# Kernel tuning notes

Hardware: AMD Instinct MI355X
Metric: run time of the kernel (lower is better)

Reference implementation:

```python
import jax, jax.numpy as jnp
import numpy as np

DIM_MODEL = 512
SCALE = DIM_MODEL ** (-0.5)


def setup_inputs() -> dict:
    key = jax.random.key(0)
    k1, k2, k3, k4 = jax.random.split(key, 4)
    n, d, c_q, h, w = 64, 512, 512, 8, 128
    t = h * w
    query = jax.random.normal(k1, (n, d, c_q), dtype=jnp.float32)
    key_t = jax.random.normal(k2, (n, d, t), dtype=jnp.float32)
    value = jax.random.normal(k3, (n, d, t), dtype=jnp.float32)
    # valid ratios in [0.5, 1.0] so every sample keeps a non-empty valid width
    valid_ratios = 0.5 + 0.5 * jax.random.uniform(k4, (n,), dtype=jnp.float32)
    return {"query": query, "key": key_t, "value": value,
            "valid_ratios": valid_ratios, "h": h, "w": w}


def reference(query, key, value, valid_ratios, h, w):
    # query: [n, d, c]; key: [n, d, t]; value: [n, d, t]; t = h*w
    q = jnp.transpose(query, (0, 2, 1))                 # [n, c, d]
    logits = jnp.einsum('ncd,ndt->nct', q, key) * SCALE  # [n, c, t]
    n, c, t = logits.shape
    # per-sample valid width: min(w, int(w * ratio + 0.5)) (truncation == floor for positive)
    valid_width = jnp.minimum(w, jnp.floor(w * valid_ratios + 0.5)).astype(jnp.int32)  # [n]
    col = jnp.arange(w, dtype=jnp.int32)
    col_mask = col[None, :] < valid_width[:, None]       # [n, w]
    logits = logits.reshape(n, c, h, w)
    logits = jnp.where(col_mask[:, None, None, :], logits, -jnp.inf)
    weights = jax.nn.softmax(logits.reshape(n, c, t), axis=2)  # [n, c, t]
    v = jnp.transpose(value, (0, 2, 1))                  # [n, t, d]
    glimpse = jnp.einsum('nct,ntd->ncd', weights, v)     # [n, c, d]
    return jnp.transpose(glimpse, (0, 2, 1))             # [n, d, c]
```

## Files before the change

kernel.cpp:

```cpp
#include <hip/hip_runtime.h>
#include <hip/hip_bf16.h>

#define NS   64
#define DDIM 512
#define CDIM 512
#define TDIM 1024
#define WW   128
#define CB   64
#define TBLK 128
#define BK   64
#define SCALE 0.04419417382415922f

typedef __attribute__((ext_vector_type(4)))  float f32x4;
typedef __attribute__((ext_vector_type(16))) float f32x16;
typedef __attribute__((ext_vector_type(4)))  short s16x4;
typedef __attribute__((ext_vector_type(8)))  short s16x8;

#define LGKM_BARRIER() asm volatile("s_waitcnt lgkmcnt(0)\n\ts_barrier" ::: "memory")

__device__ __forceinline__ unsigned short f2bf(float f) {
  unsigned int b = __float_as_uint(f);
  return (unsigned short)((b + 0x7FFFu + ((b >> 16) & 1u)) >> 16);
}
__device__ __forceinline__ float bf2f(unsigned short u) {
  return __uint_as_float(((unsigned int)u) << 16);
}

#define AS_OFF 0
#define BS_OFF 8704
#define PS_OFF 26112
#define ZA_OFF 43008
#define IZ_OFF 43264
#define SMEM_BYTES 43520

struct QKRegs { f32x4 q0, q1, ka0, ka1, kb0, kb1; };
struct VRegs  { f32x4 a0, a1, b0, b1; };

__device__ __forceinline__ void issue_qk(QKRegs& r,
                                         const float* __restrict__ qbase,
                                         const float* __restrict__ kbase,
                                         int k0, int t0,
                                         int a_mg, int a_kq, int b_tg, int b_kq) {
  const float* gq = qbase + (size_t)(k0 + 2 * a_kq) * CDIM + 4 * a_mg;
  r.q0 = *(const f32x4*)gq;
  r.q1 = *(const f32x4*)(gq + CDIM);
  const float* gk0 = kbase + (size_t)(k0 + 2 * b_kq) * TDIM + t0 + 4 * b_tg;
  const float* gk1 = gk0 + (size_t)32 * TDIM;
  r.ka0 = *(const f32x4*)gk0;
  r.ka1 = *(const f32x4*)(gk0 + TDIM);
  r.kb0 = *(const f32x4*)gk1;
  r.kb1 = *(const f32x4*)(gk1 + TDIM);
}

__device__ __forceinline__ void issue_v(VRegs& r,
                                        const float* __restrict__ vrow0,
                                        int ks, int lhi) {
  const int kk = ks * 16 + 8 * lhi;
  const float* vp0 = vrow0 + kk;
  r.a0 = *(const f32x4*)vp0;
  r.a1 = *(const f32x4*)(vp0 + 4);
  const float* vp1 = vp0 + (size_t)32 * TDIM;
  r.b0 = *(const f32x4*)vp1;
  r.b1 = *(const f32x4*)(vp1 + 4);
}

__device__ __forceinline__ s16x8 cvt_bv(const f32x4& x0, const f32x4& x1) {
  s16x8 bv;
  bv[0] = (short)f2bf(x0[0]); bv[1] = (short)f2bf(x0[1]);
  bv[2] = (short)f2bf(x0[2]); bv[3] = (short)f2bf(x0[3]);
  bv[4] = (short)f2bf(x1[0]); bv[5] = (short)f2bf(x1[1]);
  bv[6] = (short)f2bf(x1[2]); bv[7] = (short)f2bf(x1[3]);
  return bv;
}

__global__ __launch_bounds__(512, 1)
void attn_fused_kernel(const float* __restrict__ query,
                       const float* __restrict__ key,
                       const float* __restrict__ value,
                       const float* __restrict__ ratios,
                       float* __restrict__ out)
{
  __shared__ __align__(16) char smem[SMEM_BYTES];
  unsigned short* As = (unsigned short*)(smem + AS_OFF);
  unsigned short* Bs = (unsigned short*)(smem + BS_OFF);
  unsigned short* Ps = (unsigned short*)(smem + PS_OFF);
  float* Zacc = (float*)(smem + ZA_OFF);
  float* invZ = (float*)(smem + IZ_OFF);
  float* Obuf = (float*)(smem + AS_OFF);

  const int lin  = blockIdx.x + (int)gridDim.x * blockIdx.y;
  const int n    = 8 * (lin & 7) + (lin >> 6);
  const int c0   = ((lin >> 3) & 7) * CB;

  const int tid  = threadIdx.x;
  const int wave = tid >> 6;
  const int lane = tid & 63;
  const int l31  = lane & 31;
  const int lhi  = lane >> 5;

  float r = ratios[n];
  int vw = (int)floorf(128.0f * r + 0.5f);
  if (vw > 128) vw = 128;

  if (tid < 64) Zacc[tid] = 0.0f;

  const float* qbase = query + (size_t)n * DDIM * CDIM + c0;
  const float* kbase = key   + (size_t)n * DDIM * TDIM;
  const float* vbase = value + (size_t)n * DDIM * TDIM;

  f32x16 o_acc[2][2];
  #pragma unroll
  for (int a = 0; a < 2; ++a)
    #pragma unroll
    for (int b = 0; b < 2; ++b)
      #pragma unroll
      for (int i = 0; i < 16; ++i) o_acc[a][b][i] = 0.0f;

  const int p1_ct = wave & 1;
  const int p1_tt = wave >> 1;
  const int a_mg = tid & 15, a_kq = tid >> 4;
  const int b_tg = tid & 31, b_kq = tid >> 5;
  const float* vrow0_base = vbase + (size_t)(64 * wave + l31) * TDIM;

  QKRegs buf[2];
  issue_qk(buf[0], qbase, kbase, 0,  0, a_mg, a_kq, b_tg, b_kq);
  issue_qk(buf[1], qbase, kbase, BK, 0, a_mg, a_kq, b_tg, b_kq);

  LGKM_BARRIER();

  for (int tb = 0; tb < 8; ++tb) {
    const int t0 = tb * TBLK;
    f32x16 s_acc;
    #pragma unroll
    for (int i = 0; i < 16; ++i) s_acc[i] = 0.0f;

    #pragma unroll
    for (int kit = 0; kit < 8; ++kit) {
      const int g = tb * 8 + kit;
      QKRegs& rb = buf[kit & 1];

      LGKM_BARRIER();

      #pragma unroll
      for (int j = 0; j < 4; ++j) {
        unsigned int pk = (unsigned int)f2bf(rb.q0[j]) | ((unsigned int)f2bf(rb.q1[j]) << 16);
        *(unsigned int*)&As[(4 * a_mg + j) * 68 + 2 * a_kq] = pk;
      }
      #pragma unroll
      for (int j = 0; j < 4; ++j) {
        unsigned int p0 = (unsigned int)f2bf(rb.ka0[j]) | ((unsigned int)f2bf(rb.ka1[j]) << 16);
        unsigned int p1 = (unsigned int)f2bf(rb.kb0[j]) | ((unsigned int)f2bf(rb.kb1[j]) << 16);
        *(unsigned int*)&Bs[(4 * b_tg + j) * 68 + 2 * b_kq]      = p0;
        *(unsigned int*)&Bs[(4 * b_tg + j) * 68 + 2 * b_kq + 32] = p1;
      }

      {
        int gg = g + 2; if (gg > 63) gg = 63;
        issue_qk(rb, qbase, kbase, (gg & 7) * BK, (gg >> 3) * TBLK,
                 a_mg, a_kq, b_tg, b_kq);
      }

      LGKM_BARRIER();

      const int arow = (32 * p1_ct + l31) * 68;
      const int brow = (32 * p1_tt + l31) * 68;
      #pragma unroll
      for (int ks = 0; ks < 4; ++ks) {
        const int koff = ks * 16 + 8 * lhi;
        s16x4 a0 = *(const s16x4*)&As[arow + koff];
        s16x4 a1 = *(const s16x4*)&As[arow + koff + 4];
        s16x4 b0 = *(const s16x4*)&Bs[brow + koff];
        s16x4 b1 = *(const s16x4*)&Bs[brow + koff + 4];
        s16x8 av = __builtin_shufflevector(a0, a1, 0, 1, 2, 3, 4, 5, 6, 7);
        s16x8 bv = __builtin_shufflevector(b0, b1, 0, 1, 2, 3, 4, 5, 6, 7);
        s_acc = __builtin_amdgcn_mfma_f32_32x32x16_bf16(av, bv, s_acc, 0, 0, 0);
      }
    }

    {
      const int tcol = 32 * p1_tt + l31;
      const float pm = (tcol < vw) ? 1.0f : 0.0f;
      #pragma unroll
      for (int rg = 0; rg < 16; ++rg) {
        const int c_loc = 32 * p1_ct + (rg & 3) + 8 * (rg >> 2) + 4 * lhi;
        float p = pm * __expf(s_acc[rg] * SCALE);
        Ps[c_loc * 132 + tcol] = f2bf(p);
      }
    }
    LGKM_BARRIER();

    {
      const int zr = tid >> 3;
      const int zo = (tid & 7) * 16;
      float zs = 0.0f;
      #pragma unroll
      for (int j = 0; j < 16; ++j) zs += bf2f(Ps[zr * 132 + zo + j]);
      zs += __shfl_xor(zs, 1);
      zs += __shfl_xor(zs, 2);
      zs += __shfl_xor(zs, 4);
      if ((tid & 7) == 0) Zacc[zr] += zs;
    }

    {
      const float* vrow0 = vrow0_base + t0;
      VRegs vb[2];
      issue_v(vb[0], vrow0, 0, lhi);
      issue_v(vb[1], vrow0, 1, lhi);
      #pragma unroll
      for (int ks = 0; ks < 8; ++ks) {
        const int kk = ks * 16 + 8 * lhi;
        s16x8 pa[2];
        #pragma unroll
        for (int ci = 0; ci < 2; ++ci) {
          const int row = (32 * ci + l31) * 132;
          s16x4 x0 = *(const s16x4*)&Ps[row + kk];
          s16x4 x1 = *(const s16x4*)&Ps[row + kk + 4];
          pa[ci] = __builtin_shufflevector(x0, x1, 0, 1, 2, 3, 4, 5, 6, 7);
        }
        VRegs& vr = vb[ks & 1];
        s16x8 bv0 = cvt_bv(vr.a0, vr.a1);
        s16x8 bv1 = cvt_bv(vr.b0, vr.b1);
        if (ks < 6) issue_v(vr, vrow0, ks + 2, lhi);
        o_acc[0][0] = __builtin_amdgcn_mfma_f32_32x32x16_bf16(pa[0], bv0, o_acc[0][0], 0, 0, 0);
        o_acc[1][0] = __builtin_amdgcn_mfma_f32_32x32x16_bf16(pa[1], bv0, o_acc[1][0], 0, 0, 0);
        o_acc[0][1] = __builtin_amdgcn_mfma_f32_32x32x16_bf16(pa[0], bv1, o_acc[0][1], 0, 0, 0);
        o_acc[1][1] = __builtin_amdgcn_mfma_f32_32x32x16_bf16(pa[1], bv1, o_acc[1][1], 0, 0, 0);
      }
    }
  }

  LGKM_BARRIER();
  if (tid < 64) invZ[tid] = 1.0f / Zacc[tid];
  LGKM_BARRIER();

  float* outn = out + (size_t)n * DDIM * CDIM + c0;
  for (int ch = 0; ch < 4; ++ch) {
    if ((wave >> 1) == ch) {
      const int s = wave & 1;
      #pragma unroll
      for (int ci = 0; ci < 2; ++ci)
        #pragma unroll
        for (int dt = 0; dt < 2; ++dt)
          #pragma unroll
          for (int rg = 0; rg < 16; ++rg) {
            const int c_loc = 32 * ci + (rg & 3) + 8 * (rg >> 2) + 4 * lhi;
            const int ddl = 64 * s + 32 * dt + l31;
            Obuf[c_loc * 129 + ddl] = o_acc[ci][dt][rg] * invZ[c_loc];
          }
    }
    LGKM_BARRIER();
    {
      const int c = tid & 63;
      const int db = tid >> 6;
      #pragma unroll
      for (int p = 0; p < 16; ++p) {
        const int ddl = db + 8 * p;
        outn[(size_t)(128 * ch + ddl) * CDIM + c] = Obuf[c * 129 + ddl];
      }
    }
    LGKM_BARRIER();
  }
}

extern "C" void kernel_launch(void* const* d_in, const int* in_sizes, int n_in,
                              void* d_out, int out_size, void* d_ws, size_t ws_size,
                              hipStream_t stream) {
  const float* query  = (const float*)d_in[0];
  const float* key    = (const float*)d_in[1];
  const float* value  = (const float*)d_in[2];
  const float* ratios = (const float*)d_in[3];
  float* out = (float*)d_out;
  (void)in_sizes; (void)n_in; (void)out_size; (void)d_ws; (void)ws_size;
  dim3 grid(CDIM / CB, NS);
  attn_fused_kernel<<<grid, 512, 0, stream>>>(query, key, value, ratios, out);
}
```

Baseline: 545.3 us.

## Double-buffer QK LDS tiles, widen T block, accumulate softmax sums in registers

Doubles the T block from 128 to 256 so each wave computes two 32x32 score tiles per Q fragment, reusing the A operand. Q/K staging in LDS is now double-buffered, which drops one of the two barriers per k-iteration. The softmax denominator is accumulated in fp32 registers and reduced with shuffles at the end, replacing the per-block LDS re-read of the bf16 P tile. LDS use grows to about 119 KB and launch bounds now request 2 blocks per CU, which that LDS size likely cannot satisfy, so register pressure is capped with little occupancy in return.

```diff
diff --git a/kernel.cpp b/kernel.cpp
--- a/kernel.cpp
+++ b/kernel.cpp
@@ -1,13 +1,11 @@
 #include <hip/hip_runtime.h>
-#include <hip/hip_bf16.h>
 
 #define NS   64
 #define DDIM 512
 #define CDIM 512
 #define TDIM 1024
-#define WW   128
 #define CB   64
-#define TBLK 128
+#define TBLK 256
 #define BK   64
 #define SCALE 0.04419417382415922f
 
@@ -22,46 +20,32 @@
   unsigned int b = __float_as_uint(f);
   return (unsigned short)((b + 0x7FFFu + ((b >> 16) & 1u)) >> 16);
 }
-__device__ __forceinline__ float bf2f(unsigned short u) {
-  return __uint_as_float(((unsigned int)u) << 16);
-}
-
-#define AS_OFF 0
-#define BS_OFF 8704
-#define PS_OFF 26112
-#define ZA_OFF 43008
-#define IZ_OFF 43264
-#define SMEM_BYTES 43520
-
-struct QKRegs { f32x4 q0, q1, ka0, ka1, kb0, kb1; };
-struct VRegs  { f32x4 a0, a1, b0, b1; };
-
-__device__ __forceinline__ void issue_qk(QKRegs& r,
-                                         const float* __restrict__ qbase,
-                                         const float* __restrict__ kbase,
-                                         int k0, int t0,
-                                         int a_mg, int a_kq, int b_tg, int b_kq) {
-  const float* gq = qbase + (size_t)(k0 + 2 * a_kq) * CDIM + 4 * a_mg;
-  r.q0 = *(const f32x4*)gq;
-  r.q1 = *(const f32x4*)(gq + CDIM);
-  const float* gk0 = kbase + (size_t)(k0 + 2 * b_kq) * TDIM + t0 + 4 * b_tg;
-  const float* gk1 = gk0 + (size_t)32 * TDIM;
-  r.ka0 = *(const f32x4*)gk0;
-  r.ka1 = *(const f32x4*)(gk0 + TDIM);
-  r.kb0 = *(const f32x4*)gk1;
-  r.kb1 = *(const f32x4*)(gk1 + TDIM);
-}
-
-__device__ __forceinline__ void issue_v(VRegs& r,
-                                        const float* __restrict__ vrow0,
+__device__ __forceinline__ unsigned int pk2(float a, float b) {
+  return (unsigned int)f2bf(a) | ((unsigned int)f2bf(b) << 16);
+}
+
+#define AS_STRIDE 68
+#define BS_STRIDE 68
+#define PS_STRIDE 260
+#define AS0_OFF 0
+#define AS1_OFF 8704
+#define BS0_OFF 17408
+#define BS1_OFF 52224
+#define PS_OFF  87040
+#define ZP_OFF  120320
+#define IZ_OFF  121344
+#define SMEM_BYTES 121600
+
+struct Stage { f32x4 q0, q1, ka[4], kb[4]; };
+struct VRegs { f32x4 a0, a1, b0, b1; };
+
+__device__ __forceinline__ void issue_v(VRegs& r, const float* __restrict__ vrow,
                                         int ks, int lhi) {
   const int kk = ks * 16 + 8 * lhi;
-  const float* vp0 = vrow0 + kk;
-  r.a0 = *(const f32x4*)vp0;
-  r.a1 = *(const f32x4*)(vp0 + 4);
-  const float* vp1 = vp0 + (size_t)32 * TDIM;
-  r.b0 = *(const f32x4*)vp1;
-  r.b1 = *(const f32x4*)(vp1 + 4);
+  r.a0 = *(const f32x4*)(vrow + kk);
+  r.a1 = *(const f32x4*)(vrow + kk + 4);
+  r.b0 = *(const f32x4*)(vrow + (size_t)32 * TDIM + kk);
+  r.b1 = *(const f32x4*)(vrow + (size_t)32 * TDIM + kk + 4);
 }
 
 __device__ __forceinline__ s16x8 cvt_bv(const f32x4& x0, const f32x4& x1) {
@@ -73,7 +57,7 @@
   return bv;
 }
 
-__global__ __launch_bounds__(512, 1)
+__global__ __launch_bounds__(512, 2)
 void attn_fused_kernel(const float* __restrict__ query,
                        const float* __restrict__ key,
                        const float* __restrict__ value,
@@ -81,12 +65,14 @@
                        float* __restrict__ out)
 {
   __shared__ __align__(16) char smem[SMEM_BYTES];
-  unsigned short* As = (unsigned short*)(smem + AS_OFF);
-  unsigned short* Bs = (unsigned short*)(smem + BS_OFF);
+  unsigned short* Asbuf[2] = {(unsigned short*)(smem + AS0_OFF),
+                              (unsigned short*)(smem + AS1_OFF)};
+  unsigned short* Bsbuf[2] = {(unsigned short*)(smem + BS0_OFF),
+                              (unsigned short*)(smem + BS1_OFF)};
   unsigned short* Ps = (unsigned short*)(smem + PS_OFF);
-  float* Zacc = (float*)(smem + ZA_OFF);
-  float* invZ = (float*)(smem + IZ_OFF);
-  float* Obuf = (float*)(smem + AS_OFF);
+  float* Zpart = (float*)(smem + ZP_OFF);
+  float* invZ  = (float*)(smem + IZ_OFF);
+  float* Obuf  = (float*)smem;
 
   const int lin  = blockIdx.x + (int)gridDim.x * blockIdx.y;
   const int n    = 8 * (lin & 7) + (lin >> 6);
@@ -98,16 +84,22 @@
   const int l31  = lane & 31;
   const int lhi  = lane >> 5;
 
-  float r = ratios[n];
-  int vw = (int)floorf(128.0f * r + 0.5f);
+  float rr = ratios[n];
+  int vw = (int)floorf(128.0f * rr + 0.5f);
   if (vw > 128) vw = 128;
-
-  if (tid < 64) Zacc[tid] = 0.0f;
 
   const float* qbase = query + (size_t)n * DDIM * CDIM + c0;
   const float* kbase = key   + (size_t)n * DDIM * TDIM;
   const float* vbase = value + (size_t)n * DDIM * TDIM;
 
+  const int kpq = (tid & 7) + 8 * (tid >> 7);
+  const int cg  = (tid >> 3) & 15;
+  const int kpk = tid & 7;
+  const int tg  = tid >> 3;
+
+  const int ct  = wave & 1;
+  const int ttp = wave >> 1;
+
   f32x16 o_acc[2][2];
   #pragma unroll
   for (int a = 0; a < 2; ++a)
@@ -116,103 +108,108 @@
       #pragma unroll
       for (int i = 0; i < 16; ++i) o_acc[a][b][i] = 0.0f;
 
-  const int p1_ct = wave & 1;
-  const int p1_tt = wave >> 1;
-  const int a_mg = tid & 15, a_kq = tid >> 4;
-  const int b_tg = tid & 31, b_kq = tid >> 5;
-  const float* vrow0_base = vbase + (size_t)(64 * wave + l31) * TDIM;
-
-  QKRegs buf[2];
-  issue_qk(buf[0], qbase, kbase, 0,  0, a_mg, a_kq, b_tg, b_kq);
-  issue_qk(buf[1], qbase, kbase, BK, 0, a_mg, a_kq, b_tg, b_kq);
-
-  LGKM_BARRIER();
-
-  for (int tb = 0; tb < 8; ++tb) {
+  float z_loc[16];
+  #pragma unroll
+  for (int i = 0; i < 16; ++i) z_loc[i] = 0.0f;
+
+  Stage st;
+  auto issue_stage = [&](int g) {
+    const int k0 = (g & 7) * BK;
+    const int t0 = (g >> 3) * TBLK;
+    const float* gq = qbase + (size_t)(k0 + 2 * kpq) * CDIM + 4 * cg;
+    st.q0 = *(const f32x4*)gq;
+    st.q1 = *(const f32x4*)(gq + CDIM);
+    #pragma unroll
+    for (int i = 0; i < 4; ++i) {
+      const int d = k0 + 2 * (kpk + 8 * i);
+      const float* gk = kbase + (size_t)d * TDIM + t0 + 4 * tg;
+      st.ka[i] = *(const f32x4*)gk;
+      st.kb[i] = *(const f32x4*)(gk + TDIM);
+    }
+  };
+  auto write_stage = [&](int b) {
+    unsigned int* Au = (unsigned int*)Asbuf[b];
+    unsigned int* Bu = (unsigned int*)Bsbuf[b];
+    #pragma unroll
+    for (int j = 0; j < 4; ++j)
+      Au[(4 * cg + j) * (AS_STRIDE / 2) + kpq] = pk2(st.q0[j], st.q1[j]);
+    #pragma unroll
+    for (int i = 0; i < 4; ++i)
+      #pragma unroll
+      for (int j = 0; j < 4; ++j)
+        Bu[(4 * tg + j) * (BS_STRIDE / 2) + kpk + 8 * i] = pk2(st.ka[i][j], st.kb[i][j]);
+  };
+
+  issue_stage(0);
+  write_stage(0);
+  issue_stage(1);
+
+  const int arow  = (32 * ct + l31) * AS_STRIDE;
+  const int brow0 = (64 * ttp + l31) * BS_STRIDE;
+  const int brow1 = brow0 + 32 * BS_STRIDE;
+
+  for (int tb = 0; tb < 4; ++tb) {
     const int t0 = tb * TBLK;
-    f32x16 s_acc;
-    #pragma unroll
-    for (int i = 0; i < 16; ++i) s_acc[i] = 0.0f;
+    f32x16 sa[2];
+    #pragma unroll
+    for (int q = 0; q < 2; ++q)
+      #pragma unroll
+      for (int i = 0; i < 16; ++i) sa[q][i] = 0.0f;
 
     #pragma unroll
     for (int kit = 0; kit < 8; ++kit) {
       const int g = tb * 8 + kit;
-      QKRegs& rb = buf[kit & 1];
-
       LGKM_BARRIER();
-
-      #pragma unroll
-      for (int j = 0; j < 4; ++j) {
-        unsigned int pk = (unsigned int)f2bf(rb.q0[j]) | ((unsigned int)f2bf(rb.q1[j]) << 16);
-        *(unsigned int*)&As[(4 * a_mg + j) * 68 + 2 * a_kq] = pk;
-      }
-      #pragma unroll
-      for (int j = 0; j < 4; ++j) {
-        unsigned int p0 = (unsigned int)f2bf(rb.ka0[j]) | ((unsigned int)f2bf(rb.ka1[j]) << 16);
-        unsigned int p1 = (unsigned int)f2bf(rb.kb0[j]) | ((unsigned int)f2bf(rb.kb1[j]) << 16);
-        *(unsigned int*)&Bs[(4 * b_tg + j) * 68 + 2 * b_kq]      = p0;
-        *(unsigned int*)&Bs[(4 * b_tg + j) * 68 + 2 * b_kq + 32] = p1;
-      }
-
+      write_stage((kit + 1) & 1);
       {
-        int gg = g + 2; if (gg > 63) gg = 63;
-        issue_qk(rb, qbase, kbase, (gg & 7) * BK, (gg >> 3) * TBLK,
-                 a_mg, a_kq, b_tg, b_kq);
-      }
-
-      LGKM_BARRIER();
-
-      const int arow = (32 * p1_ct + l31) * 68;
-      const int brow = (32 * p1_tt + l31) * 68;
+        int gg = g + 2; if (gg > 31) gg = 31;
+        issue_stage(gg);
+      }
+      const unsigned short* Ab = Asbuf[kit & 1];
+      const unsigned short* Bb = Bsbuf[kit & 1];
       #pragma unroll
       for (int ks = 0; ks < 4; ++ks) {
         const int koff = ks * 16 + 8 * lhi;
-        s16x4 a0 = *(const s16x4*)&As[arow + koff];
-        s16x4 a1 = *(const s16x4*)&As[arow + koff + 4];
-        s16x4 b0 = *(const s16x4*)&Bs[brow + koff];
-        s16x4 b1 = *(const s16x4*)&Bs[brow + koff + 4];
+        s16x4 a0 = *(const s16x4*)&Ab[arow + koff];
+        s16x4 a1 = *(const s16x4*)&Ab[arow + koff + 4];
         s16x8 av = __builtin_shufflevector(a0, a1, 0, 1, 2, 3, 4, 5, 6, 7);
-        s16x8 bv = __builtin_shufflevector(b0, b1, 0, 1, 2, 3, 4, 5, 6, 7);
-        s_acc = __builtin_amdgcn_mfma_f32_32x32x16_bf16(av, bv, s_acc, 0, 0, 0);
-      }
-    }
+        s16x4 b00 = *(const s16x4*)&Bb[brow0 + koff];
+        s16x4 b01 = *(const s16x4*)&Bb[brow0 + koff + 4];
+        s16x8 bv0 = __builtin_shufflevector(b00, b01, 0, 1, 2, 3, 4, 5, 6, 7);
+        s16x4 b10 = *(const s16x4*)&Bb[brow1 + koff];
+        s16x4 b11 = *(const s16x4*)&Bb[brow1 + koff + 4];
+        s16x8 bv1 = __builtin_shufflevector(b10, b11, 0, 1, 2, 3, 4, 5, 6, 7);
+        sa[0] = __builtin_amdgcn_mfma_f32_32x32x16_bf16(av, bv0, sa[0], 0, 0, 0);
+        sa[1] = __builtin_amdgcn_mfma_f32_32x32x16_bf16(av, bv1, sa[1], 0, 0, 0);
+      }
+    }
+
+    #pragma unroll
+    for (int tt2 = 0; tt2 < 2; ++tt2) {
+      const int tcol = 64 * ttp + 32 * tt2 + l31;
+      const float pm = ((tcol & 127) < vw) ? 1.0f : 0.0f;
+      #pragma unroll
+      for (int rg = 0; rg < 16; ++rg) {
+        const int c_loc = 32 * ct + (rg & 3) + 8 * (rg >> 2) + 4 * lhi;
+        float p = pm * __expf(sa[tt2][rg] * SCALE);
+        Ps[c_loc * PS_STRIDE + tcol] = f2bf(p);
+        z_loc[rg] += p;
+      }
+    }
+    LGKM_BARRIER();
 
     {
-      const int tcol = 32 * p1_tt + l31;
-      const float pm = (tcol < vw) ? 1.0f : 0.0f;
-      #pragma unroll
-      for (int rg = 0; rg < 16; ++rg) {
-        const int c_loc = 32 * p1_ct + (rg & 3) + 8 * (rg >> 2) + 4 * lhi;
-        float p = pm * __expf(s_acc[rg] * SCALE);
-        Ps[c_loc * 132 + tcol] = f2bf(p);
-      }
-    }
-    LGKM_BARRIER();
-
-    {
-      const int zr = tid >> 3;
-      const int zo = (tid & 7) * 16;
-      float zs = 0.0f;
-      #pragma unroll
-      for (int j = 0; j < 16; ++j) zs += bf2f(Ps[zr * 132 + zo + j]);
-      zs += __shfl_xor(zs, 1);
-      zs += __shfl_xor(zs, 2);
-      zs += __shfl_xor(zs, 4);
-      if ((tid & 7) == 0) Zacc[zr] += zs;
-    }
-
-    {
-      const float* vrow0 = vrow0_base + t0;
+      const float* vrow = vbase + (size_t)(64 * wave + l31) * TDIM + t0;
       VRegs vb[2];
-      issue_v(vb[0], vrow0, 0, lhi);
-      issue_v(vb[1], vrow0, 1, lhi);
-      #pragma unroll
-      for (int ks = 0; ks < 8; ++ks) {
+      issue_v(vb[0], vrow, 0, lhi);
+      issue_v(vb[1], vrow, 1, lhi);
+      #pragma unroll
+      for (int ks = 0; ks < 16; ++ks) {
         const int kk = ks * 16 + 8 * lhi;
         s16x8 pa[2];
         #pragma unroll
         for (int ci = 0; ci < 2; ++ci) {
-          const int row = (32 * ci + l31) * 132;
+          const int row = (32 * ci + l31) * PS_STRIDE;
           s16x4 x0 = *(const s16x4*)&Ps[row + kk];
           s16x4 x1 = *(const s16x4*)&Ps[row + kk + 4];
           pa[ci] = __builtin_shufflevector(x0, x1, 0, 1, 2, 3, 4, 5, 6, 7);
@@ -220,7 +217,7 @@
         VRegs& vr = vb[ks & 1];
         s16x8 bv0 = cvt_bv(vr.a0, vr.a1);
         s16x8 bv1 = cvt_bv(vr.b0, vr.b1);
-        if (ks < 6) issue_v(vr, vrow0, ks + 2, lhi);
+        if (ks < 14) issue_v(vr, vrow, ks + 2, lhi);
         o_acc[0][0] = __builtin_amdgcn_mfma_f32_32x32x16_bf16(pa[0], bv0, o_acc[0][0], 0, 0, 0);
         o_acc[1][0] = __builtin_amdgcn_mfma_f32_32x32x16_bf16(pa[1], bv0, o_acc[1][0], 0, 0, 0);
         o_acc[0][1] = __builtin_amdgcn_mfma_f32_32x32x16_bf16(pa[0], bv1, o_acc[0][1], 0, 0, 0);
@@ -229,8 +226,21 @@
     }
   }
 
+  #pragma unroll
+  for (int m = 1; m <= 16; m <<= 1)
+    #pragma unroll
+    for (int rg = 0; rg < 16; ++rg)
+      z_loc[rg] += __shfl_xor(z_loc[rg], m);
+  if (l31 == 0) {
+    #pragma unroll
+    for (int rg = 0; rg < 16; ++rg) {
+      const int row = 32 * ct + (rg & 3) + 8 * (rg >> 2) + 4 * lhi;
+      Zpart[64 * ttp + row] = z_loc[rg];
+    }
+  }
   LGKM_BARRIER();
-  if (tid < 64) invZ[tid] = 1.0f / Zacc[tid];
+  if (tid < 64)
+    invZ[tid] = 1.0f / (Zpart[tid] + Zpart[64 + tid] + Zpart[128 + tid] + Zpart[192 + tid]);
   LGKM_BARRIER();
 
   float* outn = out + (size_t)n * DDIM * CDIM + c0;
```

After: 622.7 us. 14.2% more time.
